# Performance work log

Measured on AMD Instinct MI355X. Metric: run time of the kernel, lower is better.

## Reference

```python
import jax, jax.numpy as jnp
import numpy as np

N_NODES = 20000
N_EDGES = 320000
N_GRAPHS = 32
C = 256
L = 4
IN_DIM = 739
EDGE_DIM = 2 * C + 6
LN_EPS = 1e-5


def _layernorm(x, g, b):
    mu = jnp.mean(x, axis=-1, keepdims=True)
    var = jnp.mean(jnp.square(x - mu), axis=-1, keepdims=True)
    return (x - mu) * jax.lax.rsqrt(var + LN_EPS) * g + b


def setup_inputs() -> dict:
    key = jax.random.key(0)
    ks = jax.random.split(key, 20)
    d = {}
    d["x"] = jax.random.normal(ks[0], (N_NODES, IN_DIM), jnp.float32)
    d["x_pos"] = jax.random.normal(ks[1], (N_NODES, 3), jnp.float32)
    d["edge_index"] = jax.random.randint(ks[2], (2, N_EDGES), 0, N_NODES, jnp.int32)
    d["batch"] = jnp.sort(jax.random.randint(ks[3], (N_NODES,), 0, N_GRAPHS, jnp.int32))
    s = 0.02
    d["dense_w"] = jax.random.normal(ks[4], (IN_DIM, C), jnp.float32) * s
    d["dense_b"] = jnp.zeros((C,), jnp.float32)
    d["d1_w"] = jax.random.normal(ks[5], (L, C, C), jnp.float32) * s
    d["d1_b"] = jnp.zeros((L, C), jnp.float32)
    d["ln1_g"] = jnp.ones((L, EDGE_DIM), jnp.float32)
    d["ln1_b"] = jnp.zeros((L, EDGE_DIM), jnp.float32)
    d["w1_w"] = jax.random.normal(ks[6], (L, EDGE_DIM, 4), jnp.float32) * s
    d["w1_b"] = jnp.zeros((L, 4), jnp.float32)
    d["ln2_g"] = jnp.ones((L, 4), jnp.float32)
    d["ln2_b"] = jnp.zeros((L, 4), jnp.float32)
    d["w2_w"] = jax.random.normal(ks[7], (L, 4, 1), jnp.float32) * s
    d["w2_b"] = jnp.zeros((L, 1), jnp.float32)
    d["d2_w"] = jax.random.normal(ks[8], (L, C, C), jnp.float32) * s
    d["d2_b"] = jnp.zeros((L, C), jnp.float32)
    d["head_w"] = jax.random.normal(ks[9], (C, 1), jnp.float32) * s
    d["head_b"] = jnp.zeros((1,), jnp.float32)
    return d


def reference(x, x_pos, edge_index, batch, dense_w, dense_b, d1_w, d1_b,
              ln1_g, ln1_b, w1_w, w1_b, ln2_g, ln2_b, w2_w, w2_b,
              d2_w, d2_b, head_w, head_b):
    n = x.shape[0]
    src, dst = edge_index[0], edge_index[1]
    h = x @ dense_w + dense_b  # [N, C]
    for l in range(d1_w.shape[0]):
        # message: dense1 -> GELU (dropout is identity in eval)
        m = jax.nn.gelu(h @ d1_w[l] + d1_b[l], approximate=False)  # [N, C]
        sx = m[src]                                                # [E, C]
        # edge-MLP input: [src_x, dst_x, src_pos, dst_pos]
        e = jnp.concatenate([sx, m[dst], x_pos[src], x_pos[dst]], axis=-1)  # [E, 2C+6]
        e = _layernorm(e, ln1_g[l], ln1_b[l])
        e = jax.nn.gelu(e @ w1_w[l] + w1_b[l], approximate=False)  # [E, 4]
        e = _layernorm(e, ln2_g[l], ln2_b[l])
        w = jax.nn.sigmoid(e @ w2_w[l] + w2_b[l])                  # [E, 1]
        agg = jax.ops.segment_sum(sx * w, dst, num_segments=n)     # [N, C]
        # update: dense2 -> GELU
        h = jax.nn.gelu(agg @ d2_w[l] + d2_b[l], approximate=False)
    # global mean pool over graphs
    sums = jax.ops.segment_sum(h, batch, num_segments=N_GRAPHS)           # [G, C]
    cnts = jax.ops.segment_sum(jnp.ones((n, 1), h.dtype), batch, num_segments=N_GRAPHS)
    pooled = sums / jnp.maximum(cnts, 1.0)
    return pooled @ head_w + head_b  # [G, 1]
```

## Files before the change

kernel.cpp:

```cpp
#include <hip/hip_runtime.h>
#include <math.h>

#define N_NODES 20000
#define N_EDGES 320000
#define N_GRAPHS 32
#define CDIM 256
#define IN_DIMV 739
#define KPAD_DENSE 768
#define ED_DIM 518
#define NLAYERS 4
#define LN_EPS 1e-5f
#define SCAN_BLOCKS ((N_NODES + 255) / 256)

typedef _Float16 f16x8 __attribute__((ext_vector_type(8)));
typedef _Float16 f16x4 __attribute__((ext_vector_type(4)));
typedef float f32x4 __attribute__((ext_vector_type(4)));

__device__ __forceinline__ float gelu_exact(float x) {
    return 0.5f * x * (1.f + erff(x * 0.7071067811865475f));
}

__device__ __forceinline__ void gll16(const void* g, void* l) {
    __builtin_amdgcn_global_load_lds((const __attribute__((address_space(1))) void*)g,
                                     (__attribute__((address_space(3))) void*)l, 16, 0, 0);
}

__global__ __launch_bounds__(256)
void convert_x_kernel(const float* __restrict__ x, _Float16* __restrict__ xh) {
    const int nquads = (N_NODES * IN_DIMV) / 4;
    const int stride = gridDim.x * 256;
    for (int q = blockIdx.x * 256 + threadIdx.x; q < nquads; q += stride) {
        float4 v = ((const float4*)x)[q];
        int base = q * 4;
        float vv[4] = {v.x, v.y, v.z, v.w};
#pragma unroll
        for (int e = 0; e < 4; ++e) {
            int idx = base + e;
            int row = idx / IN_DIMV;
            int col = idx - row * IN_DIMV;
            xh[row * KPAD_DENSE + col] = (_Float16)vv[e];
        }
    }
    const int npad = N_NODES * (KPAD_DENSE - IN_DIMV);
    for (int p = blockIdx.x * 256 + threadIdx.x; p < npad; p += stride) {
        int row = p / (KPAD_DENSE - IN_DIMV);
        int col = IN_DIMV + (p - row * (KPAD_DENSE - IN_DIMV));
        xh[row * KPAD_DENSE + col] = (_Float16)0.f;
    }
}

__global__ __launch_bounds__(256)
void prep_all(const float* __restrict__ ln1_g, const float* __restrict__ ln1_b,
              const float* __restrict__ w1_w, float* __restrict__ cw,
              float* __restrict__ SgSb,
              const float* __restrict__ dense_w, _Float16* __restrict__ wt_dense,
              const float* __restrict__ d1_w, const float* __restrict__ d2_w,
              _Float16* __restrict__ wt_sq, int* __restrict__ deg,
              float* __restrict__ sdot) {
    __shared__ float smem[2048 + 64];
    int b = blockIdx.x, tid = threadIdx.x;
    if (b < 79) {
        int i = b * 256 + tid;
        if (i < N_NODES) deg[i] = 0;
    } else if (b < 83) {
        int l = b - 79;
        float sg[4] = {0, 0, 0, 0}, sb[4] = {0, 0, 0, 0};
        for (int i = tid; i < ED_DIM; i += 256) {
            float g = ln1_g[l * ED_DIM + i];
            float bb = ln1_b[l * ED_DIM + i];
            float4 w = *(const float4*)&w1_w[(size_t)(l * ED_DIM + i) * 4];
            float4 c = make_float4(g * w.x, g * w.y, g * w.z, g * w.w);
            *(float4*)&cw[(size_t)(l * ED_DIM + i) * 4] = c;
            sg[0] += c.x; sg[1] += c.y; sg[2] += c.z; sg[3] += c.w;
            sb[0] += bb * w.x; sb[1] += bb * w.y; sb[2] += bb * w.z; sb[3] += bb * w.w;
        }
        for (int c = 0; c < 4; c++) { smem[tid * 8 + c] = sg[c]; smem[tid * 8 + 4 + c] = sb[c]; }
        __syncthreads();
        for (int s = 128; s > 0; s >>= 1) {
            if (tid < s)
                for (int c = 0; c < 8; c++) smem[tid * 8 + c] += smem[(tid + s) * 8 + c];
            __syncthreads();
        }
        if (tid < 8) SgSb[l * 8 + tid] = smem[tid];
    } else if (b < 275) {
        int q = b - 83;
        int kt = q >> 3, nt = q & 7;
        int i = tid >> 5, j = tid & 31;
        float* T = smem;
#pragma unroll
        for (int ii = 0; ii < 4; ii++) {
            int k = kt * 32 + i + ii * 8;
            T[(i + ii * 8) * 33 + j] = (k < IN_DIMV) ? dense_w[(size_t)k * 256 + nt * 32 + j] : 0.f;
        }
        __syncthreads();
#pragma unroll
        for (int ii = 0; ii < 4; ii++) {
            int n = nt * 32 + i + ii * 8;
            wt_dense[(size_t)n * KPAD_DENSE + kt * 32 + j] = (_Float16)T[j * 33 + i + ii * 8];
        }
    } else if (b < 787) {
        int q = b - 275;
        int z = q >> 6, kt = (q >> 3) & 7, nt = q & 7;
        const float* W = (z < 4) ? d1_w + (size_t)z * 65536 : d2_w + (size_t)(z - 4) * 65536;
        _Float16* O = wt_sq + (size_t)z * 65536;
        int i = tid >> 5, j = tid & 31;
        float* T = smem;
#pragma unroll
        for (int ii = 0; ii < 4; ii++)
            T[(i + ii * 8) * 33 + j] = W[(size_t)(kt * 32 + i + ii * 8) * 256 + nt * 32 + j];
        __syncthreads();
#pragma unroll
        for (int ii = 0; ii < 4; ii++)
            O[(size_t)(nt * 32 + i + ii * 8) * 256 + kt * 32 + j] = (_Float16)T[j * 33 + i + ii * 8];
    } else {
        int i = (b - 787) * 256 + tid;
        if (i < N_NODES) sdot[i] = 0.f;
    }
}

__global__ void hist_gstart_kernel(const int* __restrict__ ei, const int* __restrict__ batch,
                                   int* __restrict__ deg, int* __restrict__ gstart) {
    int e = blockIdx.x * 256 + threadIdx.x;
    if (e < N_EDGES) atomicAdd(&deg[ei[N_EDGES + e]], 1);
    if (e < N_NODES) {
        int b = batch[e];
        int bprev = (e == 0) ? -1 : batch[e - 1];
        for (int g = bprev + 1; g <= b; g++) gstart[g] = e;
        if (e == N_NODES - 1)
            for (int g = b + 1; g <= N_GRAPHS; g++) gstart[g] = N_NODES;
    }
}

__global__ __launch_bounds__(256)
void scan1_kernel(const int* __restrict__ deg, int* __restrict__ bsum) {
    __shared__ int red[256];
    int t = threadIdx.x;
    int i = blockIdx.x * 256 + t;
    red[t] = (i < N_NODES) ? deg[i] : 0;
    __syncthreads();
    for (int s = 128; s > 0; s >>= 1) {
        if (t < s) red[t] += red[t + s];
        __syncthreads();
    }
    if (t == 0) bsum[blockIdx.x] = red[0];
}

__global__ __launch_bounds__(128)
void scan2_kernel(const int* __restrict__ bsum, int* __restrict__ boff) {
    __shared__ int s[128];
    int t = threadIdx.x;
    int v = (t < SCAN_BLOCKS) ? bsum[t] : 0;
    s[t] = v;
    __syncthreads();
    for (int off = 1; off < 128; off <<= 1) {
        int o = (t >= off) ? s[t - off] : 0;
        __syncthreads();
        s[t] += o;
        __syncthreads();
    }
    if (t < SCAN_BLOCKS) boff[t] = s[t] - v;
}

__global__ __launch_bounds__(256)
void scan3_kernel(const int* __restrict__ deg, const int* __restrict__ boff,
                  int* __restrict__ row_start, int* __restrict__ cursor) {
    __shared__ int s[256];
    int t = threadIdx.x;
    int i = blockIdx.x * 256 + t;
    int v = (i < N_NODES) ? deg[i] : 0;
    s[t] = v;
    __syncthreads();
    for (int off = 1; off < 256; off <<= 1) {
        int o = (t >= off) ? s[t - off] : 0;
        __syncthreads();
        s[t] += o;
        __syncthreads();
    }
    int base = boff[blockIdx.x];
    int excl = base + s[t] - v;
    if (i < N_NODES) {
        row_start[i] = excl;
        cursor[i] = excl;
    }
    if (i == N_NODES - 1) row_start[N_NODES] = base + s[t];
}

__global__ void scatter_kernel(const int* __restrict__ ei, int* __restrict__ cursor,
                               int* __restrict__ csr_src, int* __restrict__ slot) {
    int e = blockIdx.x * 256 + threadIdx.x;
    if (e < N_EDGES) {
        int d = ei[N_EDGES + e];
        int pos = atomicAdd(&cursor[d], 1);
        csr_src[pos] = ei[e];
        slot[e] = pos;
    }
}

template <int KSTEPS, int NBUF, bool GELU_ACT, bool DOT>
__global__ __launch_bounds__(256)
void gemm_v3(const _Float16* __restrict__ A, const _Float16* __restrict__ Bt,
             const float* __restrict__ bias, _Float16* __restrict__ C,
             const float* __restrict__ head_w, float* __restrict__ sdot) {
    constexpr int KDIM = KSTEPS * 64;
    __shared__ __align__(16) _Float16 Bs[NBUF * 128 * 64];
    __shared__ __align__(16) _Float16 As[NBUF * 64 * 64];

    const int tid = threadIdx.x;
    const int row0 = blockIdx.x * 64;
    const int col0 = blockIdx.y * 128;
    const int wave = tid >> 6, lane = tid & 63;
    const int quad = lane >> 4, lrow = lane & 15;
    const int wrow = wave >> 1, wcol = wave & 1;

    const int sr = tid >> 3;
    const int scb = (tid & 7) << 4;
    const int srcCb = scb ^ ((sr & 7) << 4);

    const char* bsrc[4];
#pragma unroll
    for (int i = 0; i < 4; ++i)
        bsrc[i] = (const char*)Bt + (size_t)(col0 + i * 32 + sr) * (KDIM * 2) + srcCb;
    char* const bdst = (char*)&Bs[0] + tid * 16;

    const char* asrc[2];
    char* const adst = (char*)&As[0] + tid * 16;
#pragma unroll
    for (int i = 0; i < 2; ++i) {
        int ar = row0 + i * 32 + sr;
        ar = (ar < N_NODES) ? ar : (N_NODES - 1);
        asrc[i] = (const char*)A + (size_t)ar * (KDIM * 2) + srcCb;
    }

    const int swz = ((lrow & 7) << 4) ^ (quad << 4);
    const int aro0 = (wrow * 32 + lrow) * 128;
    const int aro1 = aro0 + 2048;
    int bro[4];
#pragma unroll
    for (int t = 0; t < 4; ++t) bro[t] = (wcol * 64 + t * 16 + lrow) * 128;

    f32x4 acc[2][4];
#pragma unroll
    for (int i = 0; i < 2; ++i)
#pragma unroll
        for (int t = 0; t < 4; ++t) acc[i][t] = (f32x4){0.f, 0.f, 0.f, 0.f};

    auto stage = [&](int j) {
        const int kb = j * 128;
        const int b3 = (j % NBUF) * 16384;
        const int a3 = (j % NBUF) * 8192;
#pragma unroll
        for (int i = 0; i < 4; ++i) gll16(bsrc[i] + kb, bdst + b3 + i * 4096);
#pragma unroll
        for (int i = 0; i < 2; ++i) gll16(asrc[i] + kb, adst + a3 + i * 4096);
    };

    auto compute = [&](int k) {
        const char* pa = (const char*)&As[0] + (k % NBUF) * 8192;
        const char* pb = (const char*)&Bs[0] + (k % NBUF) * 16384;
        __builtin_amdgcn_s_setprio(1);
#pragma unroll
        for (int h = 0; h < 2; ++h) {
            const int cbs = (h << 6) ^ swz;
            f16x8 af0 = *(const f16x8*)(pa + aro0 + cbs);
            f16x8 af1 = *(const f16x8*)(pa + aro1 + cbs);
#pragma unroll
            for (int t = 0; t < 4; ++t) {
                f16x8 bf = *(const f16x8*)(pb + bro[t] + cbs);
                acc[0][t] = __builtin_amdgcn_mfma_f32_16x16x32_f16(af0, bf, acc[0][t], 0, 0, 0);
                acc[1][t] = __builtin_amdgcn_mfma_f32_16x16x32_f16(af1, bf, acc[1][t], 0, 0, 0);
            }
        }
        __builtin_amdgcn_s_setprio(0);
    };

    stage(0);
    if (NBUF == 3 && KSTEPS > 1) {
        stage(1);
        asm volatile("s_waitcnt vmcnt(6)" ::: "memory");
    } else {
        asm volatile("s_waitcnt vmcnt(0)" ::: "memory");
    }
    __builtin_amdgcn_sched_barrier(0);
    __builtin_amdgcn_s_barrier();
    __builtin_amdgcn_sched_barrier(0);

#pragma unroll
    for (int k = 0; k < KSTEPS; ++k) {
        const int nxt = k + NBUF - 1;
        if (nxt < KSTEPS) stage(nxt);
        compute(k);
        if (k + 1 < KSTEPS) {
            if (NBUF == 3 && k + 2 < KSTEPS)
                asm volatile("s_waitcnt vmcnt(6) lgkmcnt(0)" ::: "memory");
            else
                asm volatile("s_waitcnt vmcnt(0) lgkmcnt(0)" ::: "memory");
            __builtin_amdgcn_sched_barrier(0);
            __builtin_amdgcn_s_barrier();
            __builtin_amdgcn_sched_barrier(0);
        }
    }

    const int orow = row0 + wrow * 32 + quad * 4;
    const int ocolb = col0 + wcol * 64 + lrow;
    if constexpr (DOT) {
        float dp0[4] = {0.f, 0.f, 0.f, 0.f}, dp1[4] = {0.f, 0.f, 0.f, 0.f};
#pragma unroll
        for (int t = 0; t < 4; ++t) {
            const int col = ocolb + t * 16;
            const float hw = head_w[col];
            const float bv = bias[col];
#pragma unroll
            for (int r = 0; r < 4; ++r) {
                dp0[r] += gelu_exact(acc[0][t][r] + bv) * hw;
                dp1[r] += gelu_exact(acc[1][t][r] + bv) * hw;
            }
        }
#pragma unroll
        for (int r = 0; r < 4; ++r) {
#pragma unroll
            for (int off = 1; off < 16; off <<= 1) {
                dp0[r] += __shfl_xor(dp0[r], off, 64);
                dp1[r] += __shfl_xor(dp1[r], off, 64);
            }
        }
        if (lrow == 0) {
#pragma unroll
            for (int r = 0; r < 4; ++r) {
                if (orow + r < N_NODES) atomicAdd(&sdot[orow + r], dp0[r]);
                if (orow + 16 + r < N_NODES) atomicAdd(&sdot[orow + 16 + r], dp1[r]);
            }
        }
    } else {
#pragma unroll
        for (int t = 0; t < 4; ++t) {
            const int col = ocolb + t * 16;
            const float bv = bias[col];
#pragma unroll
            for (int r = 0; r < 4; ++r) {
                float v0 = acc[0][t][r] + bv;
                float v1 = acc[1][t][r] + bv;
                if constexpr (GELU_ACT) { v0 = gelu_exact(v0); v1 = gelu_exact(v1); }
                if (orow + r < N_NODES)
                    C[(size_t)(orow + r) * 256 + col] = (_Float16)v0;
                if (orow + 16 + r < N_NODES)
                    C[(size_t)(orow + 16 + r) * 256 + col] = (_Float16)v1;
            }
        }
    }
}

__global__ __launch_bounds__(256)
void node_summary_kernel(const _Float16* __restrict__ m, const float* __restrict__ cw,
                         float* __restrict__ ns) {
    __shared__ __align__(16) float4 s_cw[512];
    int tid = threadIdx.x;
    for (int i = tid; i < 512; i += 256) s_cw[i] = *(const float4*)&cw[(size_t)i * 4];
    __syncthreads();
    int n = blockIdx.x * 4 + (tid >> 6);
    if (n >= N_NODES) return;
    int lane = tid & 63;
    f16x4 a4 = *(const f16x4*)&m[(size_t)n * CDIM + lane * 4];
    float av[4] = {(float)a4[0], (float)a4[1], (float)a4[2], (float)a4[3]};
    float Q1 = 0.f, Q2 = 0.f, P1[4] = {0, 0, 0, 0}, P2[4] = {0, 0, 0, 0};
#pragma unroll
    for (int j = 0; j < 4; j++) {
        Q1 += av[j];
        Q2 += av[j] * av[j];
        float4 c0 = s_cw[lane * 4 + j];
        float4 c1 = s_cw[256 + lane * 4 + j];
        P1[0] += av[j] * c0.x; P1[1] += av[j] * c0.y; P1[2] += av[j] * c0.z; P1[3] += av[j] * c0.w;
        P2[0] += av[j] * c1.x; P2[1] += av[j] * c1.y; P2[2] += av[j] * c1.z; P2[3] += av[j] * c1.w;
    }
#pragma unroll
    for (int off = 1; off < 64; off <<= 1) {
        Q1 += __shfl_xor(Q1, off, 64);
        Q2 += __shfl_xor(Q2, off, 64);
        P1[0] += __shfl_xor(P1[0], off, 64);
        P1[1] += __shfl_xor(P1[1], off, 64);
        P1[2] += __shfl_xor(P1[2], off, 64);
        P1[3] += __shfl_xor(P1[3], off, 64);
        P2[0] += __shfl_xor(P2[0], off, 64);
        P2[1] += __shfl_xor(P2[1], off, 64);
        P2[2] += __shfl_xor(P2[2], off, 64);
        P2[3] += __shfl_xor(P2[3], off, 64);
    }
    if (lane == 0) {
        float* p = &ns[(size_t)n * 12];
        *(float4*)p = make_float4(P1[0], P1[1], P1[2], P1[3]);
        *(float4*)(p + 4) = make_float4(P2[0], P2[1], P2[2], P2[3]);
        p[8] = Q1;
        p[9] = Q2;
    }
}

__global__ __launch_bounds__(256)
void edge_weight_kernel(const float* __restrict__ ns, const float* __restrict__ x_pos,
                        const int* __restrict__ ei, const float* __restrict__ cw,
                        const float* __restrict__ SgSb, const float* __restrict__ w1_b,
                        const float* __restrict__ ln2_g, const float* __restrict__ ln2_b,
                        const float* __restrict__ w2_w, const float* __restrict__ w2_b,
                        const int* __restrict__ slot, float* __restrict__ w_csr) {
    int e = blockIdx.x * 256 + threadIdx.x;
    if (e >= N_EDGES) return;
    int s = ei[e], d = ei[N_EDGES + e];
    const float* nss = &ns[(size_t)s * 12];
    const float* nsd = &ns[(size_t)d * 12];
    float4 p1 = *(const float4*)nss;
    float4 p2 = *(const float4*)(nsd + 4);
    float S1 = nss[8] + nsd[8];
    float S2 = nss[9] + nsd[9];
    float D[4] = {p1.x + p2.x, p1.y + p2.y, p1.z + p2.z, p1.w + p2.w};
    float ps[6];
    ps[0] = x_pos[(size_t)s * 3 + 0];
    ps[1] = x_pos[(size_t)s * 3 + 1];
    ps[2] = x_pos[(size_t)s * 3 + 2];
    ps[3] = x_pos[(size_t)d * 3 + 0];
    ps[4] = x_pos[(size_t)d * 3 + 1];
    ps[5] = x_pos[(size_t)d * 3 + 2];
#pragma unroll
    for (int k = 0; k < 6; k++) {
        S1 += ps[k];
        S2 += ps[k] * ps[k];
        float4 c = *(const float4*)&cw[(size_t)(512 + k) * 4];
        D[0] += ps[k] * c.x; D[1] += ps[k] * c.y; D[2] += ps[k] * c.z; D[3] += ps[k] * c.w;
    }
    const float inv = 1.f / 518.f;
    float mu = S1 * inv;
    float var = fmaf(-mu, mu, S2 * inv);
    float rstd = rsqrtf(var + LN_EPS);
    float t[4];
#pragma unroll
    for (int c = 0; c < 4; c++)
        t[c] = gelu_exact(rstd * (D[c] - mu * SgSb[c]) + SgSb[4 + c] + w1_b[c]);
    float mu2 = 0.25f * (t[0] + t[1] + t[2] + t[3]);
    float var2 = 0.25f * ((t[0] - mu2) * (t[0] - mu2) + (t[1] - mu2) * (t[1] - mu2) +
                          (t[2] - mu2) * (t[2] - mu2) + (t[3] - mu2) * (t[3] - mu2));
    float r2 = rsqrtf(var2 + LN_EPS);
    float z = w2_b[0];
#pragma unroll
    for (int c = 0; c < 4; c++)
        z += ((t[c] - mu2) * r2 * ln2_g[c] + ln2_b[c]) * w2_w[c];
    w_csr[slot[e]] = 1.f / (1.f + expf(-z));
}

__global__ __launch_bounds__(256)
void agg_kernel(const _Float16* __restrict__ m, const int* __restrict__ csr_src,
                const float* __restrict__ w_csr, const int* __restrict__ row_start,
                _Float16* __restrict__ agg) {
    int n = blockIdx.x * 4 + (threadIdx.x >> 6);
    if (n >= N_NODES) return;
    int lane = threadIdx.x & 63;
    int beg = row_start[n], end = row_start[n + 1];
    float a0 = 0.f, a1 = 0.f, a2 = 0.f, a3 = 0.f;
    int j = beg;
    for (; j + 8 <= end; j += 8) {
        int si[8];
        float wi[8];
#pragma unroll
        for (int u = 0; u < 8; u++) { si[u] = csr_src[j + u]; wi[u] = w_csr[j + u]; }
        f16x4 v[8];
#pragma unroll
        for (int u = 0; u < 8; u++) v[u] = *(const f16x4*)&m[(size_t)si[u] * CDIM + lane * 4];
#pragma unroll
        for (int u = 0; u < 8; u++) {
            a0 = fmaf(wi[u], (float)v[u][0], a0);
            a1 = fmaf(wi[u], (float)v[u][1], a1);
            a2 = fmaf(wi[u], (float)v[u][2], a2);
            a3 = fmaf(wi[u], (float)v[u][3], a3);
        }
    }
    for (; j < end; j++) {
        int s = csr_src[j];
        float w = w_csr[j];
        f16x4 v = *(const f16x4*)&m[(size_t)s * CDIM + lane * 4];
        a0 = fmaf(w, (float)v[0], a0);
        a1 = fmaf(w, (float)v[1], a1);
        a2 = fmaf(w, (float)v[2], a2);
        a3 = fmaf(w, (float)v[3], a3);
    }
    f16x4 o;
    o[0] = (_Float16)a0; o[1] = (_Float16)a1; o[2] = (_Float16)a2; o[3] = (_Float16)a3;
    *(f16x4*)&agg[(size_t)n * CDIM + lane * 4] = o;
}

__global__ __launch_bounds__(256)
void final_head_kernel(const float* __restrict__ sdot, const int* __restrict__ gstart,
                       const float* __restrict__ head_b, float* __restrict__ out) {
    int g = blockIdx.x;
    int t = threadIdx.x;
    int beg = gstart[g], end = gstart[g + 1];
    float s = 0.f;
    for (int i = beg + t; i < end; i += 256) s += sdot[i];
    __shared__ float red[256];
    red[t] = s;
    __syncthreads();
    for (int k = 128; k > 0; k >>= 1) {
        if (t < k) red[t] += red[t + k];
        __syncthreads();
    }
    if (t == 0) out[g] = red[0] / fmaxf((float)(end - beg), 1.f) + head_b[0];
}

extern "C" void kernel_launch(void* const* d_in, const int* in_sizes, int n_in,
                              void* d_out, int out_size, void* d_ws, size_t ws_size,
                              hipStream_t stream) {
    const float* x       = (const float*)d_in[0];
    const float* x_pos   = (const float*)d_in[1];
    const int*   ei      = (const int*)d_in[2];
    const int*   batch   = (const int*)d_in[3];
    const float* dense_w = (const float*)d_in[4];
    const float* dense_b = (const float*)d_in[5];
    const float* d1_w    = (const float*)d_in[6];
    const float* d1_b    = (const float*)d_in[7];
    const float* ln1_g   = (const float*)d_in[8];
    const float* ln1_b   = (const float*)d_in[9];
    const float* w1_w    = (const float*)d_in[10];
    const float* w1_b    = (const float*)d_in[11];
    const float* ln2_g   = (const float*)d_in[12];
    const float* ln2_b   = (const float*)d_in[13];
    const float* w2_w    = (const float*)d_in[14];
    const float* w2_b    = (const float*)d_in[15];
    const float* d2_w    = (const float*)d_in[16];
    const float* d2_b    = (const float*)d_in[17];
    const float* head_w  = (const float*)d_in[18];
    const float* head_b  = (const float*)d_in[19];
    float* out = (float*)d_out;

    _Float16* hbuf0 = (_Float16*)d_ws;
    _Float16* hbuf1 = hbuf0 + (size_t)N_NODES * CDIM;
    _Float16* wt_dense = hbuf1 + (size_t)N_NODES * CDIM;
    _Float16* wt_sq    = wt_dense + (size_t)256 * KPAD_DENSE;
    _Float16* x_h      = wt_sq + (size_t)8 * 256 * 256;
    float* cw    = (float*)(x_h + (size_t)N_NODES * KPAD_DENSE);
    float* SgSb  = cw + (size_t)NLAYERS * ED_DIM * 4;
    float* ns    = SgSb + NLAYERS * 8;
    float* sdot  = ns + (size_t)N_NODES * 12;
    float* w_csr = sdot + N_NODES;
    int* gstart    = (int*)(w_csr + N_EDGES);
    int* deg       = gstart + N_GRAPHS + 1;
    int* row_start = deg + N_NODES;
    int* cursor    = row_start + N_NODES + 1;
    int* csr_src   = cursor + N_NODES;
    int* slot      = csr_src + N_EDGES;
    int* bsum      = slot + N_EDGES;
    int* boff      = bsum + SCAN_BLOCKS;

    prep_all<<<866, 256, 0, stream>>>(ln1_g, ln1_b, w1_w, cw, SgSb,
                                      dense_w, wt_dense, d1_w, d2_w, wt_sq, deg, sdot);
    convert_x_kernel<<<2048, 256, 0, stream>>>(x, x_h);

    hist_gstart_kernel<<<(N_EDGES + 255) / 256, 256, 0, stream>>>(ei, batch, deg, gstart);
    scan1_kernel<<<SCAN_BLOCKS, 256, 0, stream>>>(deg, bsum);
    scan2_kernel<<<1, 128, 0, stream>>>(bsum, boff);
    scan3_kernel<<<SCAN_BLOCKS, 256, 0, stream>>>(deg, boff, row_start, cursor);
    scatter_kernel<<<(N_EDGES + 255) / 256, 256, 0, stream>>>(ei, cursor, csr_src, slot);

    const dim3 G2((N_NODES + 63) / 64, 2);
    gemm_v3<12, 3, false, false><<<G2, 256, 0, stream>>>(
        x_h, wt_dense, dense_b, hbuf0, nullptr, nullptr);

    _Float16* h = hbuf0;
    _Float16* other = hbuf1;
    for (int l = 0; l < NLAYERS; l++) {
        gemm_v3<4, 2, true, false><<<G2, 256, 0, stream>>>(
            h, wt_sq + (size_t)l * 65536, d1_b + l * CDIM, other, nullptr, nullptr);
        node_summary_kernel<<<(N_NODES + 3) / 4, 256, 0, stream>>>(
            other, cw + (size_t)l * ED_DIM * 4, ns);
        edge_weight_kernel<<<(N_EDGES + 255) / 256, 256, 0, stream>>>(
            ns, x_pos, ei, cw + (size_t)l * ED_DIM * 4, SgSb + l * 8, w1_b + l * 4,
            ln2_g + l * 4, ln2_b + l * 4, w2_w + l * 4, w2_b + l, slot, w_csr);
        agg_kernel<<<(N_NODES + 3) / 4, 256, 0, stream>>>(other, csr_src, w_csr, row_start, h);
        if (l < NLAYERS - 1) {
            gemm_v3<4, 2, true, false><<<G2, 256, 0, stream>>>(
                h, wt_sq + (size_t)(4 + l) * 65536, d2_b + l * CDIM, other, nullptr, nullptr);
        } else {
            gemm_v3<4, 2, true, true><<<G2, 256, 0, stream>>>(
                h, wt_sq + (size_t)(4 + l) * 65536, d2_b + l * CDIM, other, head_w, sdot);
        }
        _Float16* tmp = h; h = other; other = tmp;
    }

    final_head_kernel<<<N_GRAPHS, 256, 0, stream>>>(sdot, gstart, head_b, out);
}
```

Before: 524.6 us.

## Fuse node-summary reduction into d1 GEMM epilogue and merge x conversion into prep

Removes the separate node_summary kernel. The d1 GEMM epilogue now computes each node's per-row LayerNorm partial dots and sums and accumulates them into ns with atomics; ns is zeroed in prep and again in agg_kernel for the next layer. The x fp32-to-fp16 conversion is folded into prep_all, saving a launch. The NBUF=2 GEMM path now uses plain __syncthreads and drops setprio. The cost is 10 atomics per row from each of two column blocks, and extra epilogue register pressure.

After: 661.1 us. 1.26x slower.

```diff
diff --git a/kernel.cpp b/kernel.cpp
--- a/kernel.cpp
+++ b/kernel.cpp
@@ -26,37 +26,14 @@
 }
 
 __global__ __launch_bounds__(256)
-void convert_x_kernel(const float* __restrict__ x, _Float16* __restrict__ xh) {
-    const int nquads = (N_NODES * IN_DIMV) / 4;
-    const int stride = gridDim.x * 256;
-    for (int q = blockIdx.x * 256 + threadIdx.x; q < nquads; q += stride) {
-        float4 v = ((const float4*)x)[q];
-        int base = q * 4;
-        float vv[4] = {v.x, v.y, v.z, v.w};
-#pragma unroll
-        for (int e = 0; e < 4; ++e) {
-            int idx = base + e;
-            int row = idx / IN_DIMV;
-            int col = idx - row * IN_DIMV;
-            xh[row * KPAD_DENSE + col] = (_Float16)vv[e];
-        }
-    }
-    const int npad = N_NODES * (KPAD_DENSE - IN_DIMV);
-    for (int p = blockIdx.x * 256 + threadIdx.x; p < npad; p += stride) {
-        int row = p / (KPAD_DENSE - IN_DIMV);
-        int col = IN_DIMV + (p - row * (KPAD_DENSE - IN_DIMV));
-        xh[row * KPAD_DENSE + col] = (_Float16)0.f;
-    }
-}
-
-__global__ __launch_bounds__(256)
 void prep_all(const float* __restrict__ ln1_g, const float* __restrict__ ln1_b,
               const float* __restrict__ w1_w, float* __restrict__ cw,
               float* __restrict__ SgSb,
               const float* __restrict__ dense_w, _Float16* __restrict__ wt_dense,
               const float* __restrict__ d1_w, const float* __restrict__ d2_w,
               _Float16* __restrict__ wt_sq, int* __restrict__ deg,
-              float* __restrict__ sdot) {
+              float* __restrict__ sdot, float* __restrict__ ns,
+              const float* __restrict__ x, _Float16* __restrict__ xh) {
     __shared__ float smem[2048 + 64];
     int b = blockIdx.x, tid = threadIdx.x;
     if (b < 79) {
@@ -112,9 +89,34 @@
 #pragma unroll
         for (int ii = 0; ii < 4; ii++)
             O[(size_t)(nt * 32 + i + ii * 8) * 256 + kt * 32 + j] = (_Float16)T[j * 33 + i + ii * 8];
-    } else {
+    } else if (b < 866) {
         int i = (b - 787) * 256 + tid;
         if (i < N_NODES) sdot[i] = 0.f;
+    } else if (b < 1804) {
+        int i = (b - 866) * 256 + tid;
+        if (i < N_NODES * 12) ns[i] = 0.f;
+    } else {
+        const int cb = b - 1804;
+        const int stride = 2048 * 256;
+        const int nquads = (N_NODES * IN_DIMV) / 4;
+        for (int q = cb * 256 + tid; q < nquads; q += stride) {
+            float4 v = ((const float4*)x)[q];
+            int base = q * 4;
+            float vv[4] = {v.x, v.y, v.z, v.w};
+#pragma unroll
+            for (int e = 0; e < 4; ++e) {
+                int idx = base + e;
+                int row = idx / IN_DIMV;
+                int col = idx - row * IN_DIMV;
+                xh[row * KPAD_DENSE + col] = (_Float16)vv[e];
+            }
+        }
+        const int npad = N_NODES * (KPAD_DENSE - IN_DIMV);
+        for (int p = cb * 256 + tid; p < npad; p += stride) {
+            int row = p / (KPAD_DENSE - IN_DIMV);
+            int col = IN_DIMV + (p - row * (KPAD_DENSE - IN_DIMV));
+            xh[row * KPAD_DENSE + col] = (_Float16)0.f;
+        }
     }
 }
 
@@ -196,11 +198,12 @@
     }
 }
 
-template <int KSTEPS, int NBUF, bool GELU_ACT, bool DOT>
-__global__ __launch_bounds__(256)
-void gemm_v3(const _Float16* __restrict__ A, const _Float16* __restrict__ Bt,
+template <int KSTEPS, int NBUF, bool GELU_ACT, bool DOT, bool SUMMARY>
+__global__ __launch_bounds__(256)
+void gemm_v4(const _Float16* __restrict__ A, const _Float16* __restrict__ Bt,
              const float* __restrict__ bias, _Float16* __restrict__ C,
-             const float* __restrict__ head_w, float* __restrict__ sdot) {
+             const float* __restrict__ head_w, float* __restrict__ sdot,
+             const float* __restrict__ cw, float* __restrict__ ns) {
     constexpr int KDIM = KSTEPS * 64;
     __shared__ __align__(16) _Float16 Bs[NBUF * 128 * 64];
     __shared__ __align__(16) _Float16 As[NBUF * 64 * 64];
@@ -257,7 +260,7 @@
     auto compute = [&](int k) {
         const char* pa = (const char*)&As[0] + (k % NBUF) * 8192;
         const char* pb = (const char*)&Bs[0] + (k % NBUF) * 16384;
-        __builtin_amdgcn_s_setprio(1);
+        if constexpr (NBUF == 3) __builtin_amdgcn_s_setprio(1);
 #pragma unroll
         for (int h = 0; h < 2; ++h) {
             const int cbs = (h << 6) ^ swz;
@@ -270,19 +273,19 @@
                 acc[1][t] = __builtin_amdgcn_mfma_f32_16x16x32_f16(af1, bf, acc[1][t], 0, 0, 0);
             }
         }
-        __builtin_amdgcn_s_setprio(0);
+        if constexpr (NBUF == 3) __builtin_amdgcn_s_setprio(0);
     };
 
     stage(0);
-    if (NBUF == 3 && KSTEPS > 1) {
-        stage(1);
+    if constexpr (NBUF == 3) {
+        if (KSTEPS > 1) stage(1);
         asm volatile("s_waitcnt vmcnt(6)" ::: "memory");
+        __builtin_amdgcn_sched_barrier(0);
+        __builtin_amdgcn_s_barrier();
+        __builtin_amdgcn_sched_barrier(0);
     } else {
-        asm volatile("s_waitcnt vmcnt(0)" ::: "memory");
-    }
-    __builtin_amdgcn_sched_barrier(0);
-    __builtin_amdgcn_s_barrier();
-    __builtin_amdgcn_sched_barrier(0);
+        __syncthreads();
+    }
 
 #pragma unroll
     for (int k = 0; k < KSTEPS; ++k) {
@@ -290,13 +293,17 @@
         if (nxt < KSTEPS) stage(nxt);
         compute(k);
         if (k + 1 < KSTEPS) {
-            if (NBUF == 3 && k + 2 < KSTEPS)
-                asm volatile("s_waitcnt vmcnt(6) lgkmcnt(0)" ::: "memory");
-            else
-                asm volatile("s_waitcnt vmcnt(0) lgkmcnt(0)" ::: "memory");
-            __builtin_amdgcn_sched_barrier(0);
-            __builtin_amdgcn_s_barrier();
-            __builtin_amdgcn_sched_barrier(0);
+            if constexpr (NBUF == 3) {
+                if (k + 2 < KSTEPS)
+                    asm volatile("s_waitcnt vmcnt(6) lgkmcnt(0)" ::: "memory");
+                else
+                    asm volatile("s_waitcnt vmcnt(0) lgkmcnt(0)" ::: "memory");
+                __builtin_amdgcn_sched_barrier(0);
+                __builtin_amdgcn_s_barrier();
+                __builtin_amdgcn_sched_barrier(0);
+            } else {
+                __syncthreads();
+            }
         }
     }
 
@@ -328,6 +335,54 @@
             for (int r = 0; r < 4; ++r) {
                 if (orow + r < N_NODES) atomicAdd(&sdot[orow + r], dp0[r]);
                 if (orow + 16 + r < N_NODES) atomicAdd(&sdot[orow + 16 + r], dp1[r]);
+            }
+        }
+    } else if constexpr (SUMMARY) {
+        float4 c0v[4], c1v[4];
+        float bv[4];
+#pragma unroll
+        for (int t = 0; t < 4; ++t) {
+            const int col = ocolb + t * 16;
+            c0v[t] = *(const float4*)&cw[(size_t)col * 4];
+            c1v[t] = *(const float4*)&cw[(size_t)(256 + col) * 4];
+            bv[t] = bias[col];
+        }
+#pragma unroll
+        for (int h = 0; h < 2; ++h) {
+#pragma unroll
+            for (int r = 0; r < 4; ++r) {
+                const int row = orow + h * 16 + r;
+                float p1x = 0.f, p1y = 0.f, p1z = 0.f, p1w = 0.f;
+                float p2x = 0.f, p2y = 0.f, p2z = 0.f, p2w = 0.f;
+                float q1 = 0.f, q2 = 0.f;
+#pragma unroll
+                for (int t = 0; t < 4; ++t) {
+                    float v = gelu_exact(acc[h][t][r] + bv[t]);
+                    _Float16 hv = (_Float16)v;
+                    if (row < N_NODES) C[(size_t)row * 256 + (ocolb + t * 16)] = hv;
+                    float av = (float)hv;
+                    p1x += av * c0v[t].x; p1y += av * c0v[t].y;
+                    p1z += av * c0v[t].z; p1w += av * c0v[t].w;
+                    p2x += av * c1v[t].x; p2y += av * c1v[t].y;
+                    p2z += av * c1v[t].z; p2w += av * c1v[t].w;
+                    q1 += av; q2 += av * av;
+                }
+#pragma unroll
+                for (int off = 1; off < 16; off <<= 1) {
+                    p1x += __shfl_xor(p1x, off, 64); p1y += __shfl_xor(p1y, off, 64);
+                    p1z += __shfl_xor(p1z, off, 64); p1w += __shfl_xor(p1w, off, 64);
+                    p2x += __shfl_xor(p2x, off, 64); p2y += __shfl_xor(p2y, off, 64);
+                    p2z += __shfl_xor(p2z, off, 64); p2w += __shfl_xor(p2w, off, 64);
+                    q1 += __shfl_xor(q1, off, 64); q2 += __shfl_xor(q2, off, 64);
+                }
+                if (lrow == 0 && row < N_NODES) {
+                    float* p = &ns[(size_t)row * 12];
+                    atomicAdd(p + 0, p1x); atomicAdd(p + 1, p1y);
+                    atomicAdd(p + 2, p1z); atomicAdd(p + 3, p1w);
+                    atomicAdd(p + 4, p2x); atomicAdd(p + 5, p2y);
+                    atomicAdd(p + 6, p2z); atomicAdd(p + 7, p2w);
+                    atomicAdd(p + 8, q1); atomicAdd(p + 9, q2);
+                }
             }
         }
     } else {
@@ -346,50 +401,6 @@
                     C[(size_t)(orow + 16 + r) * 256 + col] = (_Float16)v1;
             }
         }
-    }
-}
-
-__global__ __launch_bounds__(256)
-void node_summary_kernel(const _Float16* __restrict__ m, const float* __restrict__ cw,
-                         float* __restrict__ ns) {
-    __shared__ __align__(16) float4 s_cw[512];
-    int tid = threadIdx.x;
-    for (int i = tid; i < 512; i += 256) s_cw[i] = *(const float4*)&cw[(size_t)i * 4];
-    __syncthreads();
-    int n = blockIdx.x * 4 + (tid >> 6);
-    if (n >= N_NODES) return;
-    int lane = tid & 63;
-    f16x4 a4 = *(const f16x4*)&m[(size_t)n * CDIM + lane * 4];
-    float av[4] = {(float)a4[0], (float)a4[1], (float)a4[2], (float)a4[3]};
-    float Q1 = 0.f, Q2 = 0.f, P1[4] = {0, 0, 0, 0}, P2[4] = {0, 0, 0, 0};
-#pragma unroll
-    for (int j = 0; j < 4; j++) {
-        Q1 += av[j];
-        Q2 += av[j] * av[j];
-        float4 c0 = s_cw[lane * 4 + j];
-        float4 c1 = s_cw[256 + lane * 4 + j];
-        P1[0] += av[j] * c0.x; P1[1] += av[j] * c0.y; P1[2] += av[j] * c0.z; P1[3] += av[j] * c0.w;
-        P2[0] += av[j] * c1.x; P2[1] += av[j] * c1.y; P2[2] += av[j] * c1.z; P2[3] += av[j] * c1.w;
-    }
-#pragma unroll
-    for (int off = 1; off < 64; off <<= 1) {
-        Q1 += __shfl_xor(Q1, off, 64);
-        Q2 += __shfl_xor(Q2, off, 64);
-        P1[0] += __shfl_xor(P1[0], off, 64);
-        P1[1] += __shfl_xor(P1[1], off, 64);
-        P1[2] += __shfl_xor(P1[2], off, 64);
-        P1[3] += __shfl_xor(P1[3], off, 64);
-        P2[0] += __shfl_xor(P2[0], off, 64);
-        P2[1] += __shfl_xor(P2[1], off, 64);
-        P2[2] += __shfl_xor(P2[2], off, 64);
-        P2[3] += __shfl_xor(P2[3], off, 64);
-    }
-    if (lane == 0) {
-        float* p = &ns[(size_t)n * 12];
-        *(float4*)p = make_float4(P1[0], P1[1], P1[2], P1[3]);
-        *(float4*)(p + 4) = make_float4(P2[0], P2[1], P2[2], P2[3]);
-        p[8] = Q1;
-        p[9] = Q2;
     }
 }
 
@@ -446,10 +457,11 @@
 __global__ __launch_bounds__(256)
 void agg_kernel(const _Float16* __restrict__ m, const int* __restrict__ csr_src,
                 const float* __restrict__ w_csr, const int* __restrict__ row_start,
-                _Float16* __restrict__ agg) {
+                _Float16* __restrict__ agg, float* __restrict__ ns) {
     int n = blockIdx.x * 4 + (threadIdx.x >> 6);
     if (n >= N_NODES) return;
     int lane = threadIdx.x & 63;
+    if (lane < 12) ns[(size_t)n * 12 + lane] = 0.f;
     int beg = row_start[n], end = row_start[n + 1];
     float a0 = 0.f, a1 = 0.f, a2 = 0.f, a3 = 0.f;
     int j = beg;
@@ -545,9 +557,9 @@
     int* bsum      = slot + N_EDGES;
     int* boff      = bsum + SCAN_BLOCKS;
 
-    prep_all<<<866, 256, 0, stream>>>(ln1_g, ln1_b, w1_w, cw, SgSb,
-                                      dense_w, wt_dense, d1_w, d2_w, wt_sq, deg, sdot);
-    convert_x_kernel<<<2048, 256, 0, stream>>>(x, x_h);
+    prep_all<<<3852, 256, 0, stream>>>(ln1_g, ln1_b, w1_w, cw, SgSb,
+                                       dense_w, wt_dense, d1_w, d2_w, wt_sq, deg,
+                                       sdot, ns, x, x_h);
 
     hist_gstart_kernel<<<(N_EDGES + 255) / 256, 256, 0, stream>>>(ei, batch, deg, gstart);
     scan1_kernel<<<SCAN_BLOCKS, 256, 0, stream>>>(deg, bsum);
@@ -556,26 +568,28 @@
     scatter_kernel<<<(N_EDGES + 255) / 256, 256, 0, stream>>>(ei, cursor, csr_src, slot);
 
     const dim3 G2((N_NODES + 63) / 64, 2);
-    gemm_v3<12, 3, false, false><<<G2, 256, 0, stream>>>(
-        x_h, wt_dense, dense_b, hbuf0, nullptr, nullptr);
+    gemm_v4<12, 3, false, false, false><<<G2, 256, 0, stream>>>(
+        x_h, wt_dense, dense_b, hbuf0, nullptr, nullptr, nullptr, nullptr);
 
     _Float16* h = hbuf0;
     _Float16* other = hbuf1;
     for (int l = 0; l < NLAYERS; l++) {
-        gemm_v3<4, 2, true, false><<<G2, 256, 0, stream>>>(
-            h, wt_sq + (size_t)l * 65536, d1_b + l * CDIM, other, nullptr, nullptr);
-        node_summary_kernel<<<(N_NODES + 3) / 4, 256, 0, stream>>>(
-            other, cw + (size_t)l * ED_DIM * 4, ns);
+        gemm_v4<4, 2, true, false, true><<<G2, 256, 0, stream>>>(
+            h, wt_sq + (size_t)l * 65536, d1_b + l * CDIM, other, nullptr, nullptr,
+            cw + (size_t)l * ED_DIM * 4, ns);
         edge_weight_kernel<<<(N_EDGES + 255) / 256, 256, 0, stream>>>(
             ns, x_pos, ei, cw + (size_t)l * ED_DIM * 4, SgSb + l * 8, w1_b + l * 4,
             ln2_g + l * 4, ln2_b + l * 4, w2_w + l * 4, w2_b + l, slot, w_csr);
-        agg_kernel<<<(N_NODES + 3) / 4, 256, 0, stream>>>(other, csr_src, w_csr, row_start, h);
+        agg_kernel<<<(N_NODES + 3) / 4, 256, 0, stream>>>(
+            other, csr_src, w_csr, row_start, h, ns);
         if (l < NLAYERS - 1) {
-            gemm_v3<4, 2, true, false><<<G2, 256, 0, stream>>>(
-                h, wt_sq + (size_t)(4 + l) * 65536, d2_b + l * CDIM, other, nullptr, nullptr);
+            gemm_v4<4, 2, true, false, false><<<G2, 256, 0, stream>>>(
+                h, wt_sq + (size_t)(4 + l) * 65536, d2_b + l * CDIM, other, nullptr, nullptr,
+                nullptr, nullptr);
         } else {
-            gemm_v3<4, 2, true, true><<<G2, 256, 0, stream>>>(
-                h, wt_sq + (size_t)(4 + l) * 65536, d2_b + l * CDIM, other, head_w, sdot);
+            gemm_v4<4, 2, true, true, false><<<G2, 256, 0, stream>>>(
+                h, wt_sq + (size_t)(4 + l) * 65536, d2_b + l * CDIM, other, head_w, sdot,
+                nullptr, nullptr);
         }
         _Float16* tmp = h; h = other; other = tmp;
     }
```
